# Kernel tuning notes

Hardware: AMD Instinct MI355X
Metric: run time of the kernel (lower is better)

The kernel has to match this reference:

```python
import jax, jax.numpy as jnp
import numpy as np
from jax import lax

T = 5        # unrolled ISTA iterations (module default)
LAM = 0.1    # soft-threshold level (module default)
B, L, K = 4096, 4096, 128


def _conv1d_same(x, k):
    """TF-style SAME cross-correlation. x: [B, L], k: [K] -> [B, L]."""
    Kw = k.shape[0]
    pad_left = (Kw - 1) // 2
    pad_right = Kw - 1 - pad_left
    out = lax.conv_general_dilated(
        x[:, None, :],            # [B, 1, L]
        k[None, None, :],         # [O=1, I=1, K]
        window_strides=(1,),
        padding=[(pad_left, pad_right)],
        dimension_numbers=("NCH", "OIH", "NCH"),
    )
    return out[:, 0, :]


def setup_inputs() -> dict:
    key = jax.random.key(0)
    k1, k2 = jax.random.split(key)
    y = jax.random.normal(k1, (B, L), dtype=jnp.float32)
    thz_pulse = jax.random.normal(k2, (K,), dtype=jnp.float32)  # learned pulse (trainable)
    step_size = jnp.full((1,), 0.1, dtype=jnp.float32)          # learned step (trainable)
    return {"y": y, "thz_pulse": thz_pulse, "step_size": step_size}


def reference(y, thz_pulse, step_size):
    x = jnp.zeros_like(y)
    h = thz_pulse           # matched-filter kernel
    h_rev = thz_pulse[::-1] # time-reversed kernel (adjoint / correlation)
    s = step_size[0]
    for _ in range(T):
        conv_out = _conv1d_same(y, h)           # H y
        residual = y - conv_out                 # y - H y
        update = _conv1d_same(residual, h_rev)  # H^T residual
        x = x + s * update                      # gradient step
        x = jnp.sign(x) * jax.nn.relu(jnp.abs(x) - LAM)  # soft-threshold
    return x
```

## Files before the change

### kernel.cpp

```cpp
#include <hip/hip_runtime.h>


typedef __bf16 bf16;
typedef __bf16 bf16x4 __attribute__((ext_vector_type(4)));
typedef __bf16 bf16x8 __attribute__((ext_vector_type(8)));
typedef float f32x4 __attribute__((ext_vector_type(4)));

#define LAM 0.1f
#define RPDW 772
#define RCOLS 768
#define LDSB (16 * RPDW * 4)
#define WS_AG 0
#define WS_ZERO 80
#define WS_A1 8192
#define WS_A2 12288
#define PYE 360
#define PRE 216

__global__ __launch_bounds__(256) void ista_prep(const float* __restrict__ h,
                                                 bf16* __restrict__ ws) {
  __shared__ float hs[256];
  __shared__ float acp[256];
  __shared__ bf16 gp[384];
  const int tid = threadIdx.x;
  hs[tid] = (tid < 128) ? h[tid] : 0.f;
  gp[tid] = (bf16)0.f;
  if (tid < 128) gp[256 + tid] = (bf16)0.f;
  __syncthreads();
  const int tau = tid & 127;
  {
    const int m0 = (tid >> 7) * 64;
    float p0 = 0.f, p1 = 0.f, p2 = 0.f, p3 = 0.f;
    for (int m = m0; m < m0 + 64; m += 4) {
      p0 += hs[m] * hs[m + tau];     p1 += hs[m + 1] * hs[m + 1 + tau];
      p2 += hs[m + 2] * hs[m + 2 + tau]; p3 += hs[m + 3] * hs[m + 3 + tau];
    }
    acp[tid] = (p0 + p1) + (p2 + p3);
  }
  __syncthreads();
  if (tid < 128) {
    float ac = acp[tid] + acp[tid + 128];
    float g1 = (tau <= 63) ? hs[63 - tau] : 0.f;
    gp[145 + tau] = (bf16)(g1 - ac);
    if (tau > 0) {
      float g2 = (tau <= 64) ? hs[63 + tau] : 0.f;
      gp[145 - tau] = (bf16)(g2 - ac);
    }
  }
  __syncthreads();
  for (int i = tid; i < 1024; i += 256) {
    const int l = i >> 4, dd = i & 15;
    if (dd < 9) {
      const int o = 144 + (l >> 4) * 8 - (l & 15) + (dd - 4) * 32;
      bf16x8 a;
#pragma unroll
      for (int j = 0; j < 8; ++j) a[j] = gp[o + j];
      *reinterpret_cast<bf16x8*>(ws + WS_AG + l * 128 + dd * 8) = a;
    }
  }
  if (tid < 8) ws[WS_ZERO + tid] = (bf16)0.f;
  for (int i = tid; i < 512; i += 256) {
    const int l = i >> 3, dd = i & 7;
    if (dd < 5) {
      const int o = 127 + (l >> 4) * 8 - (l & 15) + (dd - 2) * 32;
      bf16x8 a1, a2;
#pragma unroll
      for (int j = 0; j < 8; ++j) {
        int p = o + j;
        int i1 = p - 64;
        a1[j] = ((unsigned)i1 < 128u) ? (bf16)hs[i1] : (bf16)0.f;
        int i2 = 191 - p;
        a2[j] = ((unsigned)i2 < 128u) ? (bf16)(-hs[i2]) : (bf16)0.f;
      }
      *reinterpret_cast<bf16x8*>(ws + WS_A1 + l * 64 + dd * 8) = a1;
      *reinterpret_cast<bf16x8*>(ws + WS_A2 + l * 64 + dd * 8) = a2;
    }
  }
}

__device__ __forceinline__ bf16x8 ldfragX(const float* __restrict__ rowb,
                                          int X) {
  float4 v0 = *reinterpret_cast<const float4*>(rowb + X);
  float4 v1 = *reinterpret_cast<const float4*>(rowb + X + 4);
  bf16x8 b;
  b[0] = (bf16)v0.x; b[1] = (bf16)v0.y; b[2] = (bf16)v0.z; b[3] = (bf16)v0.w;
  b[4] = (bf16)v1.x; b[5] = (bf16)v1.y; b[6] = (bf16)v1.z; b[7] = (bf16)v1.w;
  return b;
}

__global__ __launch_bounds__(256) void ista_fused(
    const float* __restrict__ y, const bf16* __restrict__ ws,
    const float* __restrict__ step, float* __restrict__ out) {
  __shared__ __align__(16) char smem[LDSB];
  const int tid = threadIdx.x;
  const int lane = tid & 63;
  const int li = lane & 15;
  const int quad = (tid >> 4) & 3;
  const int wave = tid >> 6;
  const int bid = blockIdx.x;
  const float s = step[0];

  if (bid < 512) {
    const int b0 = (bid & 255) * 16;
    const int cb = (bid >> 8) * 2048;

    bf16x8 AG[9];
#pragma unroll
    for (int dd = 0; dd < 9; ++dd)
      AG[dd] = *reinterpret_cast<const bf16x8*>(ws + WS_AG + lane * 128 + dd * 8);

    const float* zsrc = reinterpret_cast<const float*>(ws + WS_ZERO);
    const int r0 = wave * 4;
    auto issue_seg = [&](int m) {
      const int base = cb + 128 * m;
      const bool oob = ((unsigned)base >= 4096u);
      const int slotB = (((m + 6) % 6) * 128) << 2;
#pragma unroll
      for (int t = 0; t < 8; ++t) {
        const int r = r0 + (t >> 1);
        const int q = t & 1;
        const float* src =
            oob ? zsrc : (y + (size_t)(b0 + r) * 4096 + base + 64 * q + lane);
        char* dst = smem + r * (RPDW * 4) + slotB + q * 256;
        __builtin_amdgcn_global_load_lds(
            (const __attribute__((address_space(1))) void*)src,
            (__attribute__((address_space(3))) void*)dst, 4, 0, 0);
      }
    };

#pragma unroll
    for (int m = -1; m <= 3; ++m) issue_seg(m);
    asm volatile("s_waitcnt vmcnt(8)" ::: "memory");
    __builtin_amdgcn_s_barrier();
    __builtin_amdgcn_sched_barrier(0);

    const int qo = quad << 3;
    const float* rowb = reinterpret_cast<const float*>(smem) + li * RPDW;
    float* orow = out + (size_t)(b0 + li) * 4096 + cb + (quad << 2);

    bf16x8 B[9];
#pragma unroll
    for (int dd = 0; dd < 9; ++dd) {
      int col = 16 * wave + (dd - 4) * 32 + qo;
      B[dd] = ldfragX(rowb, (col + RCOLS) % RCOLS);
    }
    int o0 = 16 * wave + 160 + qo;
    int o1 = o0 + 32;

    for (int k = 0; k < 16; ++k) {
      issue_seg(k + 4);
#pragma unroll
      for (int j = 0; j < 2; ++j) {
        bf16x8 n0 = ldfragX(rowb, o0);
        bf16x8 n1 = ldfragX(rowb, o1);
        f32x4 acc0 = {0.f, 0.f, 0.f, 0.f};
        f32x4 acc1 = {0.f, 0.f, 0.f, 0.f};
        acc0 = __builtin_amdgcn_mfma_f32_16x16x32_bf16(AG[0], B[0], acc0, 0, 0, 0);
        acc1 = __builtin_amdgcn_mfma_f32_16x16x32_bf16(AG[1], B[1], acc1, 0, 0, 0);
        acc0 = __builtin_amdgcn_mfma_f32_16x16x32_bf16(AG[2], B[2], acc0, 0, 0, 0);
        acc1 = __builtin_amdgcn_mfma_f32_16x16x32_bf16(AG[3], B[3], acc1, 0, 0, 0);
        acc0 = __builtin_amdgcn_mfma_f32_16x16x32_bf16(AG[4], B[4], acc0, 0, 0, 0);
        acc1 = __builtin_amdgcn_mfma_f32_16x16x32_bf16(AG[5], B[5], acc1, 0, 0, 0);
        acc0 = __builtin_amdgcn_mfma_f32_16x16x32_bf16(AG[6], B[6], acc0, 0, 0, 0);
        acc1 = __builtin_amdgcn_mfma_f32_16x16x32_bf16(AG[7], B[7], acc1, 0, 0, 0);
        acc0 = __builtin_amdgcn_mfma_f32_16x16x32_bf16(AG[8], B[8], acc0, 0, 0, 0);
        const int tc = 128 * k + 64 * j + 16 * wave;
        const int tabs = cb + tc;
        if (tabs >= 64 && tabs < 4032) {
          float4 xv;
#pragma unroll
          for (int e = 0; e < 4; ++e) {
            float su = s * (acc0[e] + acc1[e]);
            float ax = fabsf(su) - LAM;
            ax = ax > 0.f ? ax : 0.f;
            (&xv.x)[e] = 5.f * copysignf(ax, su);
          }
          *reinterpret_cast<float4*>(orow + tc) = xv;
        }
        B[0] = B[2]; B[1] = B[3]; B[2] = B[4]; B[3] = B[5]; B[4] = B[6];
        B[5] = B[7]; B[6] = B[8]; B[7] = n0; B[8] = n1;
        o0 += 64; if (o0 >= RCOLS) o0 -= RCOLS;
        o1 += 64; if (o1 >= RCOLS) o1 -= RCOLS;
      }
      asm volatile("s_waitcnt vmcnt(8)" ::: "memory");
      __builtin_amdgcn_s_barrier();
      __builtin_amdgcn_sched_barrier(0);
    }
  } else {
    const int eid = bid - 512;
    const int chunk0 = (eid & 1) ? (4096 - 64) : 0;
    const int b0 = (eid >> 1) * 16;
    bf16* ys = reinterpret_cast<bf16*>(smem);
    bf16* rs = ys + 16 * PYE;
    const int wv = wave;

    bf16x8 A1[5], A2[5];
#pragma unroll
    for (int dd = 0; dd < 5; ++dd) {
      A1[dd] = *reinterpret_cast<const bf16x8*>(ws + WS_A1 + lane * 64 + dd * 8);
      A2[dd] = *reinterpret_cast<const bf16x8*>(ws + WS_A2 + lane * 64 + dd * 8);
    }

    {
      const int rr = tid >> 4;
      const int t = tid & 15;
      const float* yrow = y + (size_t)(b0 + rr) * 4096;
      bf16* dst = ys + rr * PYE;
#pragma unroll
      for (int k = 0; k < 6; ++k) {
        int s4 = t + 16 * k;
        if (s4 < 88) {
          int l = chunk0 - 128 + s4 * 4;
          float4 v;
          if (l >= 0 && l <= 4096 - 4) {
            v = *reinterpret_cast<const float4*>(yrow + l);
          } else {
            v.x = ((unsigned)(l + 0) < 4096u) ? yrow[l + 0] : 0.f;
            v.y = ((unsigned)(l + 1) < 4096u) ? yrow[l + 1] : 0.f;
            v.z = ((unsigned)(l + 2) < 4096u) ? yrow[l + 2] : 0.f;
            v.w = ((unsigned)(l + 3) < 4096u) ? yrow[l + 3] : 0.f;
          }
          bf16x4 bv;
          bv[0] = (bf16)v.x; bv[1] = (bf16)v.y; bv[2] = (bf16)v.z; bv[3] = (bf16)v.w;
          *reinterpret_cast<bf16x4*>(dst + s4 * 4) = bv;
        }
      }
    }
    __syncthreads();

    for (int t = wv; t < 13; t += 4) {
      const int i0 = -64 + 16 * t;
      f32x4 acc;
      {
        bf16x4 yv = *reinterpret_cast<const bf16x4*>(
            ys + li * PYE + (i0 + 128) + quad * 4);
        acc[0] = -(float)yv[0]; acc[1] = -(float)yv[1];
        acc[2] = -(float)yv[2]; acc[3] = -(float)yv[3];
      }
#pragma unroll
      for (int dd = 0; dd < 5; ++dd) {
        bf16x8 b = *reinterpret_cast<const bf16x8*>(
            ys + li * PYE + (i0 + (dd - 2) * 32 + 128) + quad * 8);
        acc = __builtin_amdgcn_mfma_f32_16x16x32_bf16(A1[dd], b, acc, 0, 0, 0);
      }
      bf16x4 rv;
#pragma unroll
      for (int e = 0; e < 4; ++e) {
        int g = chunk0 + i0 + quad * 4 + e;
        float v = ((unsigned)g < 4096u) ? acc[e] : 0.f;
        rv[e] = (bf16)v;
      }
      *reinterpret_cast<bf16x4*>(rs + li * PRE + (i0 + 64) + quad * 4) = rv;
    }
    __syncthreads();

    {
      const int i0 = 16 * wv;
      f32x4 acc = {0.f, 0.f, 0.f, 0.f};
#pragma unroll
      for (int dd = 0; dd < 5; ++dd) {
        bf16x8 b = *reinterpret_cast<const bf16x8*>(
            rs + li * PRE + (i0 + (dd - 2) * 32 + 64) + quad * 8);
        acc = __builtin_amdgcn_mfma_f32_16x16x32_bf16(A2[dd], b, acc, 0, 0, 0);
      }
      float4 xv;
#pragma unroll
      for (int e = 0; e < 4; ++e) {
        float su = s * acc[e];
        float ax = fabsf(su) - LAM;
        ax = ax > 0.f ? ax : 0.f;
        (&xv.x)[e] = 5.f * copysignf(ax, su);
      }
      *reinterpret_cast<float4*>(
          out + (size_t)(b0 + li) * 4096 + chunk0 + i0 + quad * 4) = xv;
    }
  }
}

extern "C" void kernel_launch(void* const* d_in, const int* in_sizes, int n_in,
                              void* d_out, int out_size, void* d_ws,
                              size_t ws_size, hipStream_t stream) {
  const float* y = (const float*)d_in[0];
  const float* h = (const float*)d_in[1];
  const float* s = (const float*)d_in[2];
  float* out = (float*)d_out;
  bf16* ws = (bf16*)d_ws;
  ista_prep<<<dim3(1), dim3(256), 0, stream>>>(h, ws);
  ista_fused<<<dim3(512 + 512), dim3(256), 0, stream>>>(y, ws, s, out);
}
```

Baseline: 134.6 us.

## Fuse filter prep into main kernel and double block size to 512 threads

Result: slower. 150.0 us (+11.5%).

```diff
diff --git a/kernel.cpp b/kernel.cpp
--- a/kernel.cpp
+++ b/kernel.cpp
@@ -7,76 +7,11 @@
 typedef float f32x4 __attribute__((ext_vector_type(4)));
 
 #define LAM 0.1f
-#define RPDW 772
-#define RCOLS 768
-#define LDSB (16 * RPDW * 4)
-#define WS_AG 0
-#define WS_ZERO 80
-#define WS_A1 8192
-#define WS_A2 12288
+#define RPDW 775
+#define RINGB (16 * RPDW * 4)
+#define SMEMB (RINGB + 1024 + 1024 + 768)
 #define PYE 360
 #define PRE 216
-
-__global__ __launch_bounds__(256) void ista_prep(const float* __restrict__ h,
-                                                 bf16* __restrict__ ws) {
-  __shared__ float hs[256];
-  __shared__ float acp[256];
-  __shared__ bf16 gp[384];
-  const int tid = threadIdx.x;
-  hs[tid] = (tid < 128) ? h[tid] : 0.f;
-  gp[tid] = (bf16)0.f;
-  if (tid < 128) gp[256 + tid] = (bf16)0.f;
-  __syncthreads();
-  const int tau = tid & 127;
-  {
-    const int m0 = (tid >> 7) * 64;
-    float p0 = 0.f, p1 = 0.f, p2 = 0.f, p3 = 0.f;
-    for (int m = m0; m < m0 + 64; m += 4) {
-      p0 += hs[m] * hs[m + tau];     p1 += hs[m + 1] * hs[m + 1 + tau];
-      p2 += hs[m + 2] * hs[m + 2 + tau]; p3 += hs[m + 3] * hs[m + 3 + tau];
-    }
-    acp[tid] = (p0 + p1) + (p2 + p3);
-  }
-  __syncthreads();
-  if (tid < 128) {
-    float ac = acp[tid] + acp[tid + 128];
-    float g1 = (tau <= 63) ? hs[63 - tau] : 0.f;
-    gp[145 + tau] = (bf16)(g1 - ac);
-    if (tau > 0) {
-      float g2 = (tau <= 64) ? hs[63 + tau] : 0.f;
-      gp[145 - tau] = (bf16)(g2 - ac);
-    }
-  }
-  __syncthreads();
-  for (int i = tid; i < 1024; i += 256) {
-    const int l = i >> 4, dd = i & 15;
-    if (dd < 9) {
-      const int o = 144 + (l >> 4) * 8 - (l & 15) + (dd - 4) * 32;
-      bf16x8 a;
-#pragma unroll
-      for (int j = 0; j < 8; ++j) a[j] = gp[o + j];
-      *reinterpret_cast<bf16x8*>(ws + WS_AG + l * 128 + dd * 8) = a;
-    }
-  }
-  if (tid < 8) ws[WS_ZERO + tid] = (bf16)0.f;
-  for (int i = tid; i < 512; i += 256) {
-    const int l = i >> 3, dd = i & 7;
-    if (dd < 5) {
-      const int o = 127 + (l >> 4) * 8 - (l & 15) + (dd - 2) * 32;
-      bf16x8 a1, a2;
-#pragma unroll
-      for (int j = 0; j < 8; ++j) {
-        int p = o + j;
-        int i1 = p - 64;
-        a1[j] = ((unsigned)i1 < 128u) ? (bf16)hs[i1] : (bf16)0.f;
-        int i2 = 191 - p;
-        a2[j] = ((unsigned)i2 < 128u) ? (bf16)(-hs[i2]) : (bf16)0.f;
-      }
-      *reinterpret_cast<bf16x8*>(ws + WS_A1 + l * 64 + dd * 8) = a1;
-      *reinterpret_cast<bf16x8*>(ws + WS_A2 + l * 64 + dd * 8) = a2;
-    }
-  }
-}
 
 __device__ __forceinline__ bf16x8 ldfragX(const float* __restrict__ rowb,
                                           int X) {
@@ -88,14 +23,15 @@
   return b;
 }
 
-__global__ __launch_bounds__(256) void ista_fused(
-    const float* __restrict__ y, const bf16* __restrict__ ws,
-    const float* __restrict__ step, float* __restrict__ out) {
-  __shared__ __align__(16) char smem[LDSB];
+__global__ __launch_bounds__(512) void ista_all(
+    const float* __restrict__ y, const float* __restrict__ h,
+    const float* __restrict__ zsrc, const float* __restrict__ step,
+    float* __restrict__ out) {
+  __shared__ __align__(16) char smem[SMEMB];
   const int tid = threadIdx.x;
   const int lane = tid & 63;
   const int li = lane & 15;
-  const int quad = (tid >> 4) & 3;
+  const int quad = lane >> 4;
   const int wave = tid >> 6;
   const int bid = blockIdx.x;
   const float s = step[0];
@@ -103,106 +39,162 @@
   if (bid < 512) {
     const int b0 = (bid & 255) * 16;
     const int cb = (bid >> 8) * 2048;
-
-    bf16x8 AG[9];
-#pragma unroll
-    for (int dd = 0; dd < 9; ++dd)
-      AG[dd] = *reinterpret_cast<const bf16x8*>(ws + WS_AG + lane * 128 + dd * 8);
-
-    const float* zsrc = reinterpret_cast<const float*>(ws + WS_ZERO);
-    const int r0 = wave * 4;
+    float* ringf = reinterpret_cast<float*>(smem);
+    float* hs = reinterpret_cast<float*>(smem + RINGB);
+    float* acp = hs + 256;
+    bf16* gpad = reinterpret_cast<bf16*>(acp + 256);
+
+    float hreg = 0.f;
+    if (tid < 128) hreg = h[tid];
+    asm volatile("" ::: "memory");
+
     auto issue_seg = [&](int m) {
       const int base = cb + 128 * m;
       const bool oob = ((unsigned)base >= 4096u);
-      const int slotB = (((m + 6) % 6) * 128) << 2;
-#pragma unroll
-      for (int t = 0; t < 8; ++t) {
-        const int r = r0 + (t >> 1);
+      const int slotB = (((m + 12) % 6) * 128) << 2;
+#pragma unroll
+      for (int t = 0; t < 4; ++t) {
+        const int rr = wave * 2 + (t >> 1);
         const int q = t & 1;
         const float* src =
-            oob ? zsrc : (y + (size_t)(b0 + r) * 4096 + base + 64 * q + lane);
-        char* dst = smem + r * (RPDW * 4) + slotB + q * 256;
+            oob ? (zsrc + lane)
+                : (y + (size_t)(b0 + rr) * 4096 + base + 64 * q + lane);
+        char* dst = smem + rr * (RPDW * 4) + slotB + q * 256;
         __builtin_amdgcn_global_load_lds(
             (const __attribute__((address_space(1))) void*)src,
             (__attribute__((address_space(3))) void*)dst, 4, 0, 0);
       }
     };
-
 #pragma unroll
     for (int m = -1; m <= 3; ++m) issue_seg(m);
-    asm volatile("s_waitcnt vmcnt(8)" ::: "memory");
+
+    asm volatile("s_waitcnt vmcnt(20)" ::: "memory");
+    if (tid < 256) hs[tid] = (tid < 128) ? hreg : 0.f;
+    asm volatile("s_waitcnt lgkmcnt(0)" ::: "memory");
+    __builtin_amdgcn_s_barrier();
+
+    if (tid < 256) {
+      const int tau = tid & 127;
+      const int m0 = (tid >> 7) * 64;
+      float p0 = 0.f, p1 = 0.f, p2 = 0.f, p3 = 0.f;
+      for (int m = m0; m < m0 + 64; m += 4) {
+        p0 += hs[m] * hs[m + tau];         p1 += hs[m + 1] * hs[m + 1 + tau];
+        p2 += hs[m + 2] * hs[m + 2 + tau]; p3 += hs[m + 3] * hs[m + 3 + tau];
+      }
+      acp[tid] = (p0 + p1) + (p2 + p3);
+    }
+    asm volatile("s_waitcnt lgkmcnt(0)" ::: "memory");
+    __builtin_amdgcn_s_barrier();
+
+    if (tid < 128) {
+      const int tau = tid;
+      float ac = acp[tid] + acp[tid + 128];
+      float g1 = (tau <= 63) ? hs[63 - tau] : 0.f;
+      gpad[145 + tau] = (bf16)(g1 - ac);
+      if (tau > 0) {
+        float g2 = (tau <= 64) ? hs[63 + tau] : 0.f;
+        gpad[145 - tau] = (bf16)(g2 - ac);
+      }
+    } else if (tid < 256) {
+      const int r = tid - 128;
+      if (r < 18) gpad[r] = (bf16)0.f;
+      if (273 + r < 384) gpad[273 + r] = (bf16)0.f;
+    }
+    asm volatile("s_waitcnt lgkmcnt(0)" ::: "memory");
+    __builtin_amdgcn_s_barrier();
+
+    bf16x8 AG[9];
+    {
+      const int off = 144 + quad * 8 - li;
+#pragma unroll
+      for (int dd = 0; dd < 9; ++dd) {
+        const int o = off + (dd - 4) * 32;
+        bf16x8 a;
+#pragma unroll
+        for (int j = 0; j < 8; ++j) a[j] = gpad[o + j];
+        AG[dd] = a;
+      }
+    }
+
+    asm volatile("s_waitcnt vmcnt(4)" ::: "memory");
     __builtin_amdgcn_s_barrier();
     __builtin_amdgcn_sched_barrier(0);
 
     const int qo = quad << 3;
-    const float* rowb = reinterpret_cast<const float*>(smem) + li * RPDW;
+    const float* rowb = ringf + li * RPDW;
     float* orow = out + (size_t)(b0 + li) * 4096 + cb + (quad << 2);
 
     bf16x8 B[9];
 #pragma unroll
     for (int dd = 0; dd < 9; ++dd) {
       int col = 16 * wave + (dd - 4) * 32 + qo;
-      B[dd] = ldfragX(rowb, (col + RCOLS) % RCOLS);
-    }
-    int o0 = 16 * wave + 160 + qo;
-    int o1 = o0 + 32;
+      B[dd] = ldfragX(rowb, ((col % 768) + 768) % 768);
+    }
 
     for (int k = 0; k < 16; ++k) {
       issue_seg(k + 4);
-#pragma unroll
-      for (int j = 0; j < 2; ++j) {
-        bf16x8 n0 = ldfragX(rowb, o0);
-        bf16x8 n1 = ldfragX(rowb, o1);
-        f32x4 acc0 = {0.f, 0.f, 0.f, 0.f};
-        f32x4 acc1 = {0.f, 0.f, 0.f, 0.f};
-        acc0 = __builtin_amdgcn_mfma_f32_16x16x32_bf16(AG[0], B[0], acc0, 0, 0, 0);
-        acc1 = __builtin_amdgcn_mfma_f32_16x16x32_bf16(AG[1], B[1], acc1, 0, 0, 0);
-        acc0 = __builtin_amdgcn_mfma_f32_16x16x32_bf16(AG[2], B[2], acc0, 0, 0, 0);
-        acc1 = __builtin_amdgcn_mfma_f32_16x16x32_bf16(AG[3], B[3], acc1, 0, 0, 0);
-        acc0 = __builtin_amdgcn_mfma_f32_16x16x32_bf16(AG[4], B[4], acc0, 0, 0, 0);
-        acc1 = __builtin_amdgcn_mfma_f32_16x16x32_bf16(AG[5], B[5], acc1, 0, 0, 0);
-        acc0 = __builtin_amdgcn_mfma_f32_16x16x32_bf16(AG[6], B[6], acc0, 0, 0, 0);
-        acc1 = __builtin_amdgcn_mfma_f32_16x16x32_bf16(AG[7], B[7], acc1, 0, 0, 0);
-        acc0 = __builtin_amdgcn_mfma_f32_16x16x32_bf16(AG[8], B[8], acc0, 0, 0, 0);
-        const int tc = 128 * k + 64 * j + 16 * wave;
-        const int tabs = cb + tc;
-        if (tabs >= 64 && tabs < 4032) {
-          float4 xv;
-#pragma unroll
-          for (int e = 0; e < 4; ++e) {
-            float su = s * (acc0[e] + acc1[e]);
-            float ax = fabsf(su) - LAM;
-            ax = ax > 0.f ? ax : 0.f;
-            (&xv.x)[e] = 5.f * copysignf(ax, su);
-          }
-          *reinterpret_cast<float4*>(orow + tc) = xv;
+      const int tc = 128 * k + 16 * wave;
+      if (k > 0) {
+#pragma unroll
+        for (int i = 0; i < 5; ++i) B[i] = B[i + 4];
+#pragma unroll
+        for (int dd = 5; dd < 9; ++dd) {
+          int col = tc + (dd - 4) * 32 + qo;
+          B[dd] = ldfragX(rowb, col % 768);
         }
-        B[0] = B[2]; B[1] = B[3]; B[2] = B[4]; B[3] = B[5]; B[4] = B[6];
-        B[5] = B[7]; B[6] = B[8]; B[7] = n0; B[8] = n1;
-        o0 += 64; if (o0 >= RCOLS) o0 -= RCOLS;
-        o1 += 64; if (o1 >= RCOLS) o1 -= RCOLS;
-      }
-      asm volatile("s_waitcnt vmcnt(8)" ::: "memory");
+      }
+      f32x4 acc0 = {0.f, 0.f, 0.f, 0.f};
+      f32x4 acc1 = {0.f, 0.f, 0.f, 0.f};
+      acc0 = __builtin_amdgcn_mfma_f32_16x16x32_bf16(AG[0], B[0], acc0, 0, 0, 0);
+      acc1 = __builtin_amdgcn_mfma_f32_16x16x32_bf16(AG[1], B[1], acc1, 0, 0, 0);
+      acc0 = __builtin_amdgcn_mfma_f32_16x16x32_bf16(AG[2], B[2], acc0, 0, 0, 0);
+      acc1 = __builtin_amdgcn_mfma_f32_16x16x32_bf16(AG[3], B[3], acc1, 0, 0, 0);
+      acc0 = __builtin_amdgcn_mfma_f32_16x16x32_bf16(AG[4], B[4], acc0, 0, 0, 0);
+      acc1 = __builtin_amdgcn_mfma_f32_16x16x32_bf16(AG[5], B[5], acc1, 0, 0, 0);
+      acc0 = __builtin_amdgcn_mfma_f32_16x16x32_bf16(AG[6], B[6], acc0, 0, 0, 0);
+      acc1 = __builtin_amdgcn_mfma_f32_16x16x32_bf16(AG[7], B[7], acc1, 0, 0, 0);
+      acc0 = __builtin_amdgcn_mfma_f32_16x16x32_bf16(AG[8], B[8], acc0, 0, 0, 0);
+      const int tabs = cb + tc;
+      if (tabs >= 64 && tabs < 4032) {
+        float4 xv;
+#pragma unroll
+        for (int e = 0; e < 4; ++e) {
+          float su = s * (acc0[e] + acc1[e]);
+          float ax = fabsf(su) - LAM;
+          ax = ax > 0.f ? ax : 0.f;
+          (&xv.x)[e] = 5.f * copysignf(ax, su);
+        }
+        *reinterpret_cast<float4*>(orow + tc) = xv;
+      }
+      asm volatile("s_waitcnt vmcnt(4)" ::: "memory");
       __builtin_amdgcn_s_barrier();
       __builtin_amdgcn_sched_barrier(0);
     }
   } else {
     const int eid = bid - 512;
-    const int chunk0 = (eid & 1) ? (4096 - 64) : 0;
-    const int b0 = (eid >> 1) * 16;
-    bf16* ys = reinterpret_cast<bf16*>(smem);
+    const int b0 = eid * 16;
+    const int side = tid >> 8;
+    const int wv = wave & 3;
+    const int chunk0 = side ? (4096 - 64) : 0;
+    bf16* eb = reinterpret_cast<bf16*>(smem);
+    bf16* ys = eb + side * (16 * PYE + 16 * PRE);
     bf16* rs = ys + 16 * PYE;
-    const int wv = wave;
-
-    bf16x8 A1[5], A2[5];
-#pragma unroll
-    for (int dd = 0; dd < 5; ++dd) {
-      A1[dd] = *reinterpret_cast<const bf16x8*>(ws + WS_A1 + lane * 64 + dd * 8);
-      A2[dd] = *reinterpret_cast<const bf16x8*>(ws + WS_A2 + lane * 64 + dd * 8);
-    }
-
-    {
-      const int rr = tid >> 4;
+    float* hs = reinterpret_cast<float*>(smem + 2 * (16 * PYE + 16 * PRE) * 2);
+    bf16* h1p = reinterpret_cast<bf16*>(hs + 256);
+    bf16* h2p = h1p + 256;
+
+    if (tid < 256) hs[tid] = (tid < 128) ? h[tid] : 0.f;
+    __syncthreads();
+    if (tid < 256) {
+      const int p = tid;
+      int i1 = p - 64;
+      h1p[p] = ((unsigned)i1 < 128u) ? (bf16)hs[i1] : (bf16)0.f;
+      int i2 = 191 - p;
+      h2p[p] = ((unsigned)i2 < 128u) ? (bf16)(-hs[i2]) : (bf16)0.f;
+    }
+
+    {
+      const int rr = (tid & 255) >> 4;
       const int t = tid & 15;
       const float* yrow = y + (size_t)(b0 + rr) * 4096;
       bf16* dst = ys + rr * PYE;
@@ -228,6 +220,19 @@
     }
     __syncthreads();
 
+    bf16x8 A1[5], A2[5];
+    {
+      const int off = 127 + quad * 8 - li;
+#pragma unroll
+      for (int dd = 0; dd < 5; ++dd) {
+        const int o = off + (dd - 2) * 32;
+        bf16x8 a1, a2;
+#pragma unroll
+        for (int j = 0; j < 8; ++j) { a1[j] = h1p[o + j]; a2[j] = h2p[o + j]; }
+        A1[dd] = a1; A2[dd] = a2;
+      }
+    }
+
     for (int t = wv; t < 13; t += 4) {
       const int i0 = -64 + 16 * t;
       f32x4 acc;
@@ -284,7 +289,7 @@
   const float* h = (const float*)d_in[1];
   const float* s = (const float*)d_in[2];
   float* out = (float*)d_out;
-  bf16* ws = (bf16*)d_ws;
-  ista_prep<<<dim3(1), dim3(256), 0, stream>>>(h, ws);
-  ista_fused<<<dim3(512 + 512), dim3(256), 0, stream>>>(y, ws, s, out);
+  hipMemsetAsync(d_ws, 0, 256, stream);
+  ista_all<<<dim3(512 + 256), dim3(512), 0, stream>>>(
+      y, h, (const float*)d_ws, s, out);
 }
```
